# Kernel tuning notes

Measured on AMD Instinct MI355X. Metric: run time of the kernel, lower is better.

## Reference

```python
import jax, jax.numpy as jnp
import numpy as np

N_HEADS = 4
N_GROUPS = 32
EPS = 1e-5


def setup_inputs() -> dict:
    key = jax.random.key(0)
    ks = jax.random.split(key, 6)
    c = 512
    x = jax.random.normal(ks[0], (4, c, 64, 64), dtype=jnp.float32)
    # conv1x1 weights ~ kaiming-ish scale
    s = 1.0 / np.sqrt(c)
    wq = jax.random.normal(ks[1], (c, c), dtype=jnp.float32) * s
    wk = jax.random.normal(ks[2], (c, c), dtype=jnp.float32) * s
    wv = jax.random.normal(ks[3], (c, c), dtype=jnp.float32) * s
    wp = jax.random.normal(ks[4], (c, c), dtype=jnp.float32) * s
    zeros = jnp.zeros((c,), dtype=jnp.float32)
    return {
        "x": x,
        "gn_w": jnp.ones((c,), dtype=jnp.float32), "gn_b": zeros,
        "wq": wq, "bq": zeros, "wk": wk, "bk": zeros,
        "wv": wv, "bv": zeros, "wp": wp, "bp": zeros,
    }


def _group_norm(x, w, b):
    bsz, c, h, wd = x.shape
    xg = x.reshape(bsz, N_GROUPS, c // N_GROUPS, h, wd)
    mean = xg.mean(axis=(2, 3, 4), keepdims=True)
    var = xg.var(axis=(2, 3, 4), keepdims=True)
    xg = (xg - mean) * jax.lax.rsqrt(var + EPS)
    x = xg.reshape(bsz, c, h, wd)
    return x * w[None, :, None, None] + b[None, :, None, None]


def _conv1x1(x, w, b):
    # x: (b,c,h,w), w: (out,in) -> (b,out,h,w)
    return jnp.einsum('bchw,oc->bohw', x, w) + b[None, :, None, None]


def reference(x, gn_w, gn_b, wq, bq, wk, bk, wv, bv, wp, bp):
    bsz, c, h, wd = x.shape
    hd = c // N_HEADS
    hw = h * wd
    x_n = _group_norm(x, gn_w, gn_b)
    q = _conv1x1(x_n, wq, bq)
    k = _conv1x1(x_n, wk, bk)
    v = _conv1x1(x_n, wv, bv)

    def to_heads(t):
        # (b,c,h,w) -> (b, n_heads, hw, head_dim)
        return t.reshape(bsz, N_HEADS, hd, hw).transpose(0, 1, 3, 2)

    q, k, v = to_heads(q), to_heads(k), to_heads(v)
    scale = hd ** (-0.5)
    attn = jnp.einsum('bhqd,bhkd->bhqk', q, k) * scale  # (b,H,hw,hw)
    attn = jax.nn.softmax(attn, axis=-1)
    out = jnp.einsum('bhqk,bhkd->bhqd', attn, v)
    out = out.transpose(0, 1, 3, 2).reshape(bsz, c, h, wd)
    out = _conv1x1(out, wp, bp)
    return x + out
```

## Files before the change

kernel.cpp:

```cpp
#include <hip/hip_runtime.h>
#include <math.h>

typedef __attribute__((ext_vector_type(8))) short short8;
typedef __attribute__((ext_vector_type(4))) float floatx4;
typedef __attribute__((ext_vector_type(8))) unsigned short ushort8v;
typedef __attribute__((ext_vector_type(4))) unsigned short ushort4v;

#define HW 4096
#define CCH 512
#define NB 4
#define NH 4
#define HD 128

__device__ __forceinline__ unsigned short f2bf(float f) {
    union { float f; unsigned int u; } c; c.f = f;
    unsigned int u = c.u;
    u += 0x7FFFu + ((u >> 16) & 1u);
    return (unsigned short)(u >> 16);
}

__global__ void conv_w(const float* __restrict__ w0, const float* __restrict__ w1,
                       const float* __restrict__ w2, const float* __restrict__ w3,
                       unsigned short* __restrict__ dst) {
    const float* src = blockIdx.y == 0 ? w0 : blockIdx.y == 1 ? w1 : blockIdx.y == 2 ? w2 : w3;
    unsigned short* d = dst + (size_t)blockIdx.y * 262144;
    int i = blockIdx.x * 256 + threadIdx.x;
    float4 v = ((const float4*)src)[i];
    ushort4v o;
    o[0] = f2bf(v.x); o[1] = f2bf(v.y); o[2] = f2bf(v.z); o[3] = f2bf(v.w);
    ((ushort4v*)d)[i] = o;
}

__global__ void gn_stats(const float* __restrict__ x, float* __restrict__ stats) {
    int bg = blockIdx.x;
    int b = bg >> 5, g = bg & 31;
    const float4* p = (const float4*)(x + ((size_t)b * CCH + g * 16) * HW);
    float s = 0.f, ss = 0.f;
    for (int i = threadIdx.x; i < 16384; i += 256) {
        float4 v = p[i];
        s  += v.x + v.y + v.z + v.w;
        ss += v.x * v.x + v.y * v.y + v.z * v.z + v.w * v.w;
    }
    #pragma unroll
    for (int off = 32; off > 0; off >>= 1) {
        s  += __shfl_down(s, off, 64);
        ss += __shfl_down(ss, off, 64);
    }
    __shared__ float sm[4], sm2[4];
    int wid = threadIdx.x >> 6;
    if ((threadIdx.x & 63) == 0) { sm[wid] = s; sm2[wid] = ss; }
    __syncthreads();
    if (threadIdx.x == 0) {
        float ts = sm[0] + sm[1] + sm[2] + sm[3];
        float tss = sm2[0] + sm2[1] + sm2[2] + sm2[3];
        float mean = ts * (1.f / 65536.f);
        float var = tss * (1.f / 65536.f) - mean * mean;
        stats[bg * 2] = mean;
        stats[bg * 2 + 1] = rsqrtf(var + 1e-5f);
    }
}

__global__ void gn_apply(const float* __restrict__ x, const float* __restrict__ gnw,
                         const float* __restrict__ gnb, const float* __restrict__ stats,
                         unsigned short* __restrict__ xt) {
    int s = blockIdx.x * 256 + threadIdx.x;
    int g = blockIdx.y, b = blockIdx.z;
    float mean = stats[(b * 32 + g) * 2];
    float rstd = stats[(b * 32 + g) * 2 + 1];
    const float* xb = x + ((size_t)b * CCH + g * 16) * HW + s;
    unsigned short outv[16];
    #pragma unroll
    for (int cl = 0; cl < 16; cl++) {
        int c = g * 16 + cl;
        float v = xb[(size_t)cl * HW];
        v = (v - mean) * rstd * gnw[c] + gnb[c];
        outv[cl] = f2bf(v);
    }
    unsigned short* dst = xt + ((size_t)b * HW + s) * CCH + g * 16;
    *(ushort8v*)dst       = *(ushort8v*)&outv[0];
    *(ushort8v*)(dst + 8) = *(ushort8v*)&outv[8];
}

#define LDP 72
template <int MODE>
__global__ __launch_bounds__(256, 2) void gemm_nt(
    const unsigned short* __restrict__ A, long long aStride,
    const unsigned short* __restrict__ Bm, long long bStride,
    const float* __restrict__ bias, float scale,
    const float* __restrict__ resid, long long rStride,
    void* __restrict__ Cp, long long cStride, int ldc) {
    __shared__ unsigned short lA[128 * LDP];
    __shared__ unsigned short lB[128 * LDP];
    const int tid = threadIdx.x;
    const int lane = tid & 63;
    const int wid = tid >> 6;
    const int z = blockIdx.z;
    const unsigned short* Ab = A + (size_t)z * aStride + (size_t)blockIdx.x * 128 * 512;
    const unsigned short* Bb = Bm + (size_t)z * bStride + (size_t)blockIdx.y * 128 * 512;

    floatx4 acc[4][4];
    #pragma unroll
    for (int i = 0; i < 4; i++)
        #pragma unroll
        for (int j = 0; j < 4; j++) acc[i][j] = (floatx4)0.f;

    const int wm = (wid >> 1) * 64;
    const int wn = (wid & 1) * 64;
    const int l15 = lane & 15;
    const int l4 = lane >> 4;

    for (int k0 = 0; k0 < 512; k0 += 64) {
        #pragma unroll
        for (int i = 0; i < 4; i++) {
            int idx = i * 256 + tid;
            int row = idx >> 3;
            int kc = (idx & 7) * 8;
            *(ushort8v*)&lA[row * LDP + kc] = *(const ushort8v*)&Ab[(size_t)row * 512 + k0 + kc];
            *(ushort8v*)&lB[row * LDP + kc] = *(const ushort8v*)&Bb[(size_t)row * 512 + k0 + kc];
        }
        __syncthreads();
        #pragma unroll
        for (int kk = 0; kk < 2; kk++) {
            short8 af[4], bf[4];
            #pragma unroll
            for (int i = 0; i < 4; i++)
                af[i] = *(const short8*)&lA[(wm + i * 16 + l15) * LDP + kk * 32 + l4 * 8];
            #pragma unroll
            for (int j = 0; j < 4; j++)
                bf[j] = *(const short8*)&lB[(wn + j * 16 + l15) * LDP + kk * 32 + l4 * 8];
            #pragma unroll
            for (int i = 0; i < 4; i++)
                #pragma unroll
                for (int j = 0; j < 4; j++)
                    acc[i][j] = __builtin_amdgcn_mfma_f32_16x16x32_bf16(af[i], bf[j], acc[i][j], 0, 0, 0);
        }
        __syncthreads();
    }

    long long m0 = (long long)blockIdx.x * 128 + wm;
    long long n0 = (long long)blockIdx.y * 128 + wn;
    if (MODE == 0) {
        unsigned short* C = (unsigned short*)Cp + (size_t)z * cStride;
        #pragma unroll
        for (int i = 0; i < 4; i++)
            #pragma unroll
            for (int j = 0; j < 4; j++) {
                long long col = n0 + j * 16 + l15;
                float bv = bias[col];
                #pragma unroll
                for (int r = 0; r < 4; r++) {
                    long long row = m0 + i * 16 + l4 * 4 + r;
                    C[row * ldc + col] = f2bf((acc[i][j][r] + bv) * scale);
                }
            }
    } else if (MODE == 1) {
        float* C = (float*)Cp + (size_t)z * cStride;
        const float* R = resid + (size_t)z * rStride;
        #pragma unroll
        for (int i = 0; i < 4; i++)
            #pragma unroll
            for (int j = 0; j < 4; j++)
                #pragma unroll
                for (int r = 0; r < 4; r++) {
                    long long row = m0 + i * 16 + l4 * 4 + r;
                    long long col = n0 + j * 16 + l15;
                    C[row * ldc + col] = acc[i][j][r] + bias[row] + R[row * ldc + col];
                }
    } else {
        unsigned short* C = (unsigned short*)Cp + (size_t)z * cStride;
        #pragma unroll
        for (int i = 0; i < 4; i++)
            #pragma unroll
            for (int j = 0; j < 4; j++)
                #pragma unroll
                for (int r = 0; r < 4; r++) {
                    long long row = m0 + i * 16 + l4 * 4 + r;
                    long long col = n0 + j * 16 + l15;
                    C[row * ldc + col] = f2bf(acc[i][j][r] + bias[row]);
                }
    }
}

#define LQP 136
#define LTP 72
__global__ __launch_bounds__(256, 2) void attn_kern(
    const unsigned short* __restrict__ Qb, const unsigned short* __restrict__ Kb,
    const unsigned short* __restrict__ Vt, unsigned short* __restrict__ Ob) {
    __shared__ unsigned short lk[2][64 * LQP];
    __shared__ unsigned short lvt[2][128 * LTP];
    const int tid = threadIdx.x;
    const int lane = tid & 63;
    const int w = tid >> 6;
    const int l15 = lane & 15, l4 = lane >> 4;
    const int q0 = blockIdx.x * 128;
    const int h = blockIdx.y, b = blockIdx.z;
    const size_t headOff = (size_t)h * HD;
    const size_t batchRow = (size_t)b * HW;
    const unsigned short* VtB = Vt + ((size_t)b * CCH + headOff) * HW;

    short8 qf[2][4];
    #pragma unroll
    for (int i = 0; i < 2; i++)
        #pragma unroll
        for (int kk = 0; kk < 4; kk++)
            qf[i][kk] = *(const short8*)&Qb[(batchRow + q0 + w * 32 + i * 16 + l15) * 512
                                            + headOff + kk * 32 + l4 * 8];

    short8 onesf;
    #pragma unroll
    for (int e = 0; e < 8; e++) onesf[e] = (short)0x3F80;

    floatx4 acc_o[2][8];
    floatx4 acc_l[2];
    #pragma unroll
    for (int i = 0; i < 2; i++) {
        acc_l[i] = (floatx4)0.f;
        #pragma unroll
        for (int j = 0; j < 8; j++) acc_o[i][j] = (floatx4)0.f;
    }

    ushort8v kreg[4], vreg[4];
    #pragma unroll
    for (int i = 0; i < 4; i++) {
        int idx = i * 256 + tid;
        kreg[i] = *(const ushort8v*)&Kb[(batchRow + (idx >> 4)) * 512 + headOff + (idx & 15) * 8];
        vreg[i] = *(const ushort8v*)&VtB[(size_t)(idx >> 3) * HW + (idx & 7) * 8];
    }
    #pragma unroll
    for (int i = 0; i < 4; i++) {
        int idx = i * 256 + tid;
        *(ushort8v*)&lk[0][(idx >> 4) * LQP + (idx & 15) * 8] = kreg[i];
        *(ushort8v*)&lvt[0][(idx >> 3) * LTP + (idx & 7) * 8] = vreg[i];
    }
    __syncthreads();

    int cur = 0;
    for (int kt = 0; kt < 64; kt++) {
        const unsigned short* lkc  = lk[cur];
        const unsigned short* lvtc = lvt[cur];

        if (kt < 63) {
            int t0n = (kt + 1) * 64;
            #pragma unroll
            for (int i = 0; i < 4; i++) {
                int idx = i * 256 + tid;
                kreg[i] = *(const ushort8v*)&Kb[(batchRow + t0n + (idx >> 4)) * 512 + headOff + (idx & 15) * 8];
                vreg[i] = *(const ushort8v*)&VtB[(size_t)(idx >> 3) * HW + t0n + (idx & 7) * 8];
            }
        }

        floatx4 sa[4][2];
        #pragma unroll
        for (int j = 0; j < 4; j++)
            #pragma unroll
            for (int i = 0; i < 2; i++) sa[j][i] = (floatx4)0.f;
        __builtin_amdgcn_s_setprio(1);
        #pragma unroll
        for (int kk = 0; kk < 4; kk++) {
            short8 kf[4];
            #pragma unroll
            for (int j = 0; j < 4; j++)
                kf[j] = *(const short8*)&lkc[(j * 16 + l15) * LQP + kk * 32 + l4 * 8];
            #pragma unroll
            for (int j = 0; j < 4; j++)
                #pragma unroll
                for (int i = 0; i < 2; i++)
                    sa[j][i] = __builtin_amdgcn_mfma_f32_16x16x32_bf16(kf[j], qf[i][kk], sa[j][i], 0, 0, 0);
        }
        __builtin_amdgcn_s_setprio(0);

        #pragma unroll
        for (int j = 0; j < 4; j++)
            #pragma unroll
            for (int i = 0; i < 2; i++)
                #pragma unroll
                for (int r = 0; r < 4; r++)
                    sa[j][i][r] = __builtin_amdgcn_exp2f(sa[j][i][r]);

        short8 pa[2][2];
        #pragma unroll
        for (int i = 0; i < 2; i++)
            #pragma unroll
            for (int ts = 0; ts < 2; ts++) {
                union { unsigned int u[4]; short8 s8; } pk;
                asm("v_cvt_pk_bf16_f32 %0, %1, %2" : "=v"(pk.u[0])
                    : "v"(sa[2 * ts][i][0]), "v"(sa[2 * ts][i][1]));
                asm("v_cvt_pk_bf16_f32 %0, %1, %2" : "=v"(pk.u[1])
                    : "v"(sa[2 * ts][i][2]), "v"(sa[2 * ts][i][3]));
                asm("v_cvt_pk_bf16_f32 %0, %1, %2" : "=v"(pk.u[2])
                    : "v"(sa[2 * ts + 1][i][0]), "v"(sa[2 * ts + 1][i][1]));
                asm("v_cvt_pk_bf16_f32 %0, %1, %2" : "=v"(pk.u[3])
                    : "v"(sa[2 * ts + 1][i][2]), "v"(sa[2 * ts + 1][i][3]));
                pa[i][ts] = pk.s8;
            }

        __builtin_amdgcn_s_setprio(1);
        #pragma unroll
        for (int ts = 0; ts < 2; ts++) {
            #pragma unroll
            for (int i = 0; i < 2; i++)
                acc_l[i] = __builtin_amdgcn_mfma_f32_16x16x32_bf16(pa[i][ts], onesf, acc_l[i], 0, 0, 0);
            #pragma unroll
            for (int dj = 0; dj < 8; dj++) {
                const unsigned short* vp = &lvtc[(dj * 16 + l15) * LTP + ts * 32 + l4 * 4];
                union { ushort4v h[2]; short8 s8; } vv;
                vv.h[0] = *(const ushort4v*)vp;
                vv.h[1] = *(const ushort4v*)(vp + 16);
                #pragma unroll
                for (int i = 0; i < 2; i++)
                    acc_o[i][dj] = __builtin_amdgcn_mfma_f32_16x16x32_bf16(pa[i][ts], vv.s8, acc_o[i][dj], 0, 0, 0);
            }
        }
        __builtin_amdgcn_s_setprio(0);

        if (kt < 63) {
            int nxt = cur ^ 1;
            #pragma unroll
            for (int i = 0; i < 4; i++) {
                int idx = i * 256 + tid;
                *(ushort8v*)&lk[nxt][(idx >> 4) * LQP + (idx & 15) * 8] = kreg[i];
                *(ushort8v*)&lvt[nxt][(idx >> 3) * LTP + (idx & 7) * 8] = vreg[i];
            }
            __syncthreads();
            cur = nxt;
        }
    }

    #pragma unroll
    for (int i = 0; i < 2; i++)
        #pragma unroll
        for (int r = 0; r < 4; r++) {
            float rl = 1.f / acc_l[i][r];
            size_t row = batchRow + q0 + w * 32 + i * 16 + l4 * 4 + r;
            #pragma unroll
            for (int dj = 0; dj < 8; dj++)
                Ob[row * 512 + headOff + dj * 16 + l15] = f2bf(acc_o[i][dj][r] * rl);
        }
}

extern "C" void kernel_launch(void* const* d_in, const int* in_sizes, int n_in,
                              void* d_out, int out_size, void* d_ws, size_t ws_size,
                              hipStream_t stream) {
    const float* x   = (const float*)d_in[0];
    const float* gnw = (const float*)d_in[1];
    const float* gnb = (const float*)d_in[2];
    const float* wq  = (const float*)d_in[3];
    const float* bq  = (const float*)d_in[4];
    const float* wk  = (const float*)d_in[5];
    const float* bk  = (const float*)d_in[6];
    const float* wv  = (const float*)d_in[7];
    const float* bv  = (const float*)d_in[8];
    const float* wp  = (const float*)d_in[9];
    const float* bp  = (const float*)d_in[10];
    float* out = (float*)d_out;

    const size_t NE = (size_t)NB * HW * CCH;
    unsigned short* ws16 = (unsigned short*)d_ws;
    unsigned short* XT = ws16;
    unsigned short* Qb = ws16 + NE;
    unsigned short* Kb = ws16 + 2 * NE;
    unsigned short* Vt = ws16 + 3 * NE;
    unsigned short* Wb = ws16 + 4 * NE;
    float* stats = (float*)(ws16 + 4 * NE + 4 * 262144);

    const float qscale = 0.08838834764831845f * 1.4426950408889634f;

    conv_w<<<dim3(256, 4), 256, 0, stream>>>(wq, wk, wv, wp, Wb);
    gn_stats<<<128, 256, 0, stream>>>(x, stats);
    gn_apply<<<dim3(16, 32, 4), 256, 0, stream>>>(x, gnw, gnb, stats, XT);

    gemm_nt<0><<<dim3(128, 4, 1), 256, 0, stream>>>(XT, 0, Wb + 0 * 262144, 0, bq, qscale, nullptr, 0, Qb, 0, 512);
    gemm_nt<0><<<dim3(128, 4, 1), 256, 0, stream>>>(XT, 0, Wb + 1 * 262144, 0, bk, 1.f, nullptr, 0, Kb, 0, 512);
    gemm_nt<2><<<dim3(4, 32, 4), 256, 0, stream>>>(Wb + 2 * 262144, 0, XT, (long long)HW * 512, bv, 1.f,
                                                   nullptr, 0, Vt, (long long)CCH * HW, HW);

    unsigned short* Ob = XT;
    attn_kern<<<dim3(32, NH, NB), 256, 0, stream>>>(Qb, Kb, Vt, Ob);

    gemm_nt<1><<<dim3(4, 32, 4), 256, 0, stream>>>(Wb + 3 * 262144, 0, Ob, (long long)HW * 512, bp, 1.f,
                                                   x, (long long)CCH * HW, out, (long long)CCH * HW, HW);
}
```

Measured before the change: 346.9 us.

## Switch attention kernel MFMAs from 16x16x32 to 32x32x16 bf16 tiles

Rewrites the attention inner loops to use 32x32x16 bf16 MFMA instructions, with each wave owning a 32-query tile. P fragments are rearranged from the S accumulator layout using v_permlane32_swap. The goal is fewer MFMA issues, fewer LDS reads per FLOP and better operand reuse, at the cost of larger accumulator register footprints and extra permute instructions.

```diff
diff --git a/kernel.cpp b/kernel.cpp
--- a/kernel.cpp
+++ b/kernel.cpp
@@ -3,6 +3,7 @@
 
 typedef __attribute__((ext_vector_type(8))) short short8;
 typedef __attribute__((ext_vector_type(4))) float floatx4;
+typedef __attribute__((ext_vector_type(16))) float floatx16;
 typedef __attribute__((ext_vector_type(8))) unsigned short ushort8v;
 typedef __attribute__((ext_vector_type(4))) unsigned short ushort4v;
 
@@ -191,33 +192,29 @@
     const int tid = threadIdx.x;
     const int lane = tid & 63;
     const int w = tid >> 6;
-    const int l15 = lane & 15, l4 = lane >> 4;
+    const int l31 = lane & 31;
+    const int l1 = lane >> 5;
     const int q0 = blockIdx.x * 128;
     const int h = blockIdx.y, b = blockIdx.z;
     const size_t headOff = (size_t)h * HD;
     const size_t batchRow = (size_t)b * HW;
     const unsigned short* VtB = Vt + ((size_t)b * CCH + headOff) * HW;
 
-    short8 qf[2][4];
-    #pragma unroll
-    for (int i = 0; i < 2; i++)
-        #pragma unroll
-        for (int kk = 0; kk < 4; kk++)
-            qf[i][kk] = *(const short8*)&Qb[(batchRow + q0 + w * 32 + i * 16 + l15) * 512
-                                            + headOff + kk * 32 + l4 * 8];
+    short8 qf[8];
+    #pragma unroll
+    for (int kd = 0; kd < 8; kd++)
+        qf[kd] = *(const short8*)&Qb[(batchRow + q0 + w * 32 + l31) * 512
+                                     + headOff + kd * 16 + l1 * 8];
 
     short8 onesf;
     #pragma unroll
     for (int e = 0; e < 8; e++) onesf[e] = (short)0x3F80;
 
-    floatx4 acc_o[2][8];
-    floatx4 acc_l[2];
-    #pragma unroll
-    for (int i = 0; i < 2; i++) {
-        acc_l[i] = (floatx4)0.f;
-        #pragma unroll
-        for (int j = 0; j < 8; j++) acc_o[i][j] = (floatx4)0.f;
-    }
+    floatx16 acc_o[4];
+    floatx16 acc_l;
+    acc_l = (floatx16)0.f;
+    #pragma unroll
+    for (int dj = 0; dj < 4; dj++) acc_o[dj] = (floatx16)0.f;
 
     ushort8v kreg[4], vreg[4];
     #pragma unroll
@@ -249,66 +246,56 @@
             }
         }
 
-        floatx4 sa[4][2];
-        #pragma unroll
-        for (int j = 0; j < 4; j++)
-            #pragma unroll
-            for (int i = 0; i < 2; i++) sa[j][i] = (floatx4)0.f;
+        floatx16 sa[2];
+        sa[0] = (floatx16)0.f;
+        sa[1] = (floatx16)0.f;
         __builtin_amdgcn_s_setprio(1);
         #pragma unroll
-        for (int kk = 0; kk < 4; kk++) {
-            short8 kf[4];
-            #pragma unroll
-            for (int j = 0; j < 4; j++)
-                kf[j] = *(const short8*)&lkc[(j * 16 + l15) * LQP + kk * 32 + l4 * 8];
-            #pragma unroll
-            for (int j = 0; j < 4; j++)
-                #pragma unroll
-                for (int i = 0; i < 2; i++)
-                    sa[j][i] = __builtin_amdgcn_mfma_f32_16x16x32_bf16(kf[j], qf[i][kk], sa[j][i], 0, 0, 0);
+        for (int kd = 0; kd < 8; kd++) {
+            short8 kf0 = *(const short8*)&lkc[(l31) * LQP + kd * 16 + l1 * 8];
+            short8 kf1 = *(const short8*)&lkc[(32 + l31) * LQP + kd * 16 + l1 * 8];
+            sa[0] = __builtin_amdgcn_mfma_f32_32x32x16_bf16(kf0, qf[kd], sa[0], 0, 0, 0);
+            sa[1] = __builtin_amdgcn_mfma_f32_32x32x16_bf16(kf1, qf[kd], sa[1], 0, 0, 0);
         }
         __builtin_amdgcn_s_setprio(0);
 
         #pragma unroll
-        for (int j = 0; j < 4; j++)
-            #pragma unroll
-            for (int i = 0; i < 2; i++)
-                #pragma unroll
-                for (int r = 0; r < 4; r++)
-                    sa[j][i][r] = __builtin_amdgcn_exp2f(sa[j][i][r]);
-
-        short8 pa[2][2];
-        #pragma unroll
-        for (int i = 0; i < 2; i++)
-            #pragma unroll
-            for (int ts = 0; ts < 2; ts++) {
-                union { unsigned int u[4]; short8 s8; } pk;
-                asm("v_cvt_pk_bf16_f32 %0, %1, %2" : "=v"(pk.u[0])
-                    : "v"(sa[2 * ts][i][0]), "v"(sa[2 * ts][i][1]));
-                asm("v_cvt_pk_bf16_f32 %0, %1, %2" : "=v"(pk.u[1])
-                    : "v"(sa[2 * ts][i][2]), "v"(sa[2 * ts][i][3]));
-                asm("v_cvt_pk_bf16_f32 %0, %1, %2" : "=v"(pk.u[2])
-                    : "v"(sa[2 * ts + 1][i][0]), "v"(sa[2 * ts + 1][i][1]));
-                asm("v_cvt_pk_bf16_f32 %0, %1, %2" : "=v"(pk.u[3])
-                    : "v"(sa[2 * ts + 1][i][2]), "v"(sa[2 * ts + 1][i][3]));
-                pa[i][ts] = pk.s8;
-            }
+        for (int tb = 0; tb < 2; tb++)
+            #pragma unroll
+            for (int r = 0; r < 16; r++)
+                sa[tb][r] = __builtin_amdgcn_exp2f(sa[tb][r]);
+
+        short8 paf[4];
+        #pragma unroll
+        for (int tb = 0; tb < 2; tb++) {
+            unsigned int wv[4][2];
+            #pragma unroll
+            for (int g = 0; g < 4; g++) {
+                asm("v_cvt_pk_bf16_f32 %0, %1, %2" : "=v"(wv[g][0])
+                    : "v"(sa[tb][4 * g + 0]), "v"(sa[tb][4 * g + 1]));
+                asm("v_cvt_pk_bf16_f32 %0, %1, %2" : "=v"(wv[g][1])
+                    : "v"(sa[tb][4 * g + 2]), "v"(sa[tb][4 * g + 3]));
+            }
+            #pragma unroll
+            for (int hh = 0; hh < 2; hh++) {
+                unsigned int a0 = wv[2 * hh][0], b0 = wv[2 * hh + 1][0];
+                unsigned int a1 = wv[2 * hh][1], b1 = wv[2 * hh + 1][1];
+                asm("v_permlane32_swap_b32 %0, %1" : "+v"(a0), "+v"(b0));
+                asm("v_permlane32_swap_b32 %0, %1" : "+v"(a1), "+v"(b1));
+                union { unsigned int u[4]; short8 s8; } f;
+                f.u[0] = a0; f.u[1] = a1; f.u[2] = b0; f.u[3] = b1;
+                paf[2 * tb + hh] = f.s8;
+            }
+        }
 
         __builtin_amdgcn_s_setprio(1);
         #pragma unroll
-        for (int ts = 0; ts < 2; ts++) {
-            #pragma unroll
-            for (int i = 0; i < 2; i++)
-                acc_l[i] = __builtin_amdgcn_mfma_f32_16x16x32_bf16(pa[i][ts], onesf, acc_l[i], 0, 0, 0);
-            #pragma unroll
-            for (int dj = 0; dj < 8; dj++) {
-                const unsigned short* vp = &lvtc[(dj * 16 + l15) * LTP + ts * 32 + l4 * 4];
-                union { ushort4v h[2]; short8 s8; } vv;
-                vv.h[0] = *(const ushort4v*)vp;
-                vv.h[1] = *(const ushort4v*)(vp + 16);
-                #pragma unroll
-                for (int i = 0; i < 2; i++)
-                    acc_o[i][dj] = __builtin_amdgcn_mfma_f32_16x16x32_bf16(pa[i][ts], vv.s8, acc_o[i][dj], 0, 0, 0);
+        for (int tw = 0; tw < 4; tw++) {
+            acc_l = __builtin_amdgcn_mfma_f32_32x32x16_bf16(paf[tw], onesf, acc_l, 0, 0, 0);
+            #pragma unroll
+            for (int dj = 0; dj < 4; dj++) {
+                short8 vv = *(const short8*)&lvtc[(dj * 32 + l31) * LTP + tw * 16 + l1 * 8];
+                acc_o[dj] = __builtin_amdgcn_mfma_f32_32x32x16_bf16(paf[tw], vv, acc_o[dj], 0, 0, 0);
             }
         }
         __builtin_amdgcn_s_setprio(0);
@@ -327,14 +314,16 @@
     }
 
     #pragma unroll
-    for (int i = 0; i < 2; i++)
-        #pragma unroll
-        for (int r = 0; r < 4; r++) {
-            float rl = 1.f / acc_l[i][r];
-            size_t row = batchRow + q0 + w * 32 + i * 16 + l4 * 4 + r;
-            #pragma unroll
-            for (int dj = 0; dj < 8; dj++)
-                Ob[row * 512 + headOff + dj * 16 + l15] = f2bf(acc_o[i][dj][r] * rl);
+    for (int g = 0; g < 4; g++)
+        #pragma unroll
+        for (int p = 0; p < 4; p++) {
+            int reg = 4 * g + p;
+            float rl = 1.f / acc_l[reg];
+            int qr = p + 8 * g + 4 * l1;
+            size_t row = batchRow + q0 + w * 32 + qr;
+            #pragma unroll
+            for (int dj = 0; dj < 4; dj++)
+                Ob[row * 512 + headOff + dj * 32 + l31] = f2bf(acc_o[dj][reg] * rl);
         }
 }
 
```

Measured after the change: 355.9 us. 2.6% more time.
